# Kernel optimization log

Measured on AMD Instinct MI355X. Metric: run time of the kernel, lower is better.

The kernel has to match this reference:

```python
import jax, jax.numpy as jnp
import numpy as np

EDGE_FEAT_DIM = 128
N_HEADS = 8


def setup_inputs() -> dict:
    key = jax.random.key(0)
    k1, k2, k3, k4 = jax.random.split(key, 4)
    E = 131072
    N = 4096
    edge_index = jax.random.randint(k1, (2, E), 0, N, dtype=jnp.int64)
    edge_attr = jax.random.normal(k2, (E, EDGE_FEAT_DIM), dtype=jnp.float32)
    # Linear(edge_feat_dim, n_heads) params (PyTorch default init scale)
    bound = 1.0 / np.sqrt(EDGE_FEAT_DIM)
    W = jax.random.uniform(k3, (EDGE_FEAT_DIM, N_HEADS), jnp.float32, -bound, bound)
    b = jax.random.uniform(k4, (N_HEADS,), jnp.float32, -bound, bound)
    return {"edge_index": edge_index, "edge_attr": edge_attr, "num_nodes": N,
            "W": W, "b": b}


def reference(edge_index, edge_attr, num_nodes, W, b):
    N = num_nodes
    # proj: (E, n_heads) — small GEMM
    proj = edge_attr @ W + b
    i = edge_index[0]
    j = edge_index[1]
    # In-range mask (original skips out-of-range indices; here all in-range,
    # but keep the semantics faithful).
    valid = (i >= 0) & (i < N) & (j >= 0) & (j < N)
    proj = jnp.where(valid[:, None], proj, 0.0)
    i = jnp.clip(i, 0, N - 1)
    j = jnp.clip(j, 0, N - 1)
    # Scatter-add into dense (N, N, n_heads) bias
    bias = jnp.zeros((N, N, proj.shape[-1]), dtype=proj.dtype)
    bias = bias.at[i, j].add(proj)
    return bias
```

## Files before the change

### kernel.cpp

```cpp
#include <hip/hip_runtime.h>


__global__ __launch_bounds__(256) void efe_scatter_kernel(
    const int* __restrict__ ei,
    const float* __restrict__ attr,
    const int* __restrict__ nn,
    const float* __restrict__ Wm,
    const float* __restrict__ bv,
    float* __restrict__ out,
    int E)
{
    const int N = nn[0];
    const int tid    = blockIdx.x * blockDim.x + threadIdx.x;
    const int wave   = tid >> 6;
    const int lane   = threadIdx.x & 63;
    const int lg     = lane & 15;
    const int sub    = lane >> 4;
    const int nwaves = (gridDim.x * blockDim.x) >> 6;

    float w[2][4][8];
#pragma unroll
    for (int half = 0; half < 2; ++half)
#pragma unroll
        for (int c = 0; c < 4; ++c) {
            const int k = half * 64 + lg * 4 + c;
#pragma unroll
            for (int h = 0; h < 8; ++h) w[half][c][h] = Wm[k * 8 + h];
        }
    float bh[8];
#pragma unroll
    for (int h = 0; h < 8; ++h) bh[h] = bv[h];

    const int nquads = (E + 3) >> 2;
    for (int q = wave; q < nquads; q += nwaves) {
        const int e = q * 4 + sub;
        float acc[8];
#pragma unroll
        for (int h = 0; h < 8; ++h) acc[h] = 0.f;

        const bool live = (e < E);
        if (live) {
            const float4* row = (const float4*)(attr + (size_t)e * 128);
#pragma unroll
            for (int half = 0; half < 2; ++half) {
                const float4 v = row[half * 16 + lg];
#pragma unroll
                for (int h = 0; h < 8; ++h)
                    acc[h] += v.x * w[half][0][h] + v.y * w[half][1][h]
                            + v.z * w[half][2][h] + v.w * w[half][3][h];
            }
        }
#pragma unroll
        for (int d = 1; d < 16; d <<= 1)
#pragma unroll
            for (int h = 0; h < 8; ++h)
                acc[h] += __shfl_xor(acc[h], d, 64);

        if (live && lg < 8) {
            const int i = ei[e];
            const int j = ei[E + e];
            if (i >= 0 && i < N && j >= 0 && j < N) {
                float v = acc[0] + bh[0];
#pragma unroll
                for (int h = 1; h < 8; ++h) {
                    const float cand = acc[h] + bh[h];
                    v = (lg == h) ? cand : v;
                }
                atomicAdd(out + (((size_t)i * N + j) << 3) + lg, v);
            }
        }
    }
}

extern "C" void kernel_launch(void* const* d_in, const int* in_sizes, int n_in,
                              void* d_out, int out_size, void* d_ws, size_t ws_size,
                              hipStream_t stream) {
    const int*   ei   = (const int*)d_in[0];
    const float* attr = (const float*)d_in[1];
    const int*   nn   = (const int*)d_in[2];
    const float* Wm   = (const float*)d_in[3];
    const float* bv   = (const float*)d_in[4];
    float*       out  = (float*)d_out;

    const int E = in_sizes[0] / 2;

    hipMemsetAsync(d_out, 0, (size_t)out_size * sizeof(float), stream);

    efe_scatter_kernel<<<2048, 256, 0, stream>>>(ei, attr, nn, Wm, bv, out, E);
}
```

Measured before the change: 128.5 us.

## Bin edges by output chunk and fuse zero-fill with scatter accumulation

Replaces the full-output memset and scattered global atomics with a two-pass scheme. The first kernel computes the projections into a workspace and bins edge ids into 1024-cell chunks using per-chunk counters. The second kernel writes each output chunk exactly once, accumulating binned contributions in registers and handling overflow with atomics. This removes the separate memset pass and most atomics on the large 512MB output. In exchange it needs workspace, more kernels, and a serial per-block record loop, and the overflow path scans every overflow record in every block.

```diff
diff --git a/kernel.cpp b/kernel.cpp
--- a/kernel.cpp
+++ b/kernel.cpp
@@ -1,13 +1,21 @@
 #include <hip/hip_runtime.h>
-
-
-__global__ __launch_bounds__(256) void efe_scatter_kernel(
+#include <math.h>
+
+
+#define CHUNK_CELLS 1024
+#define BIN_CAP     64
+
+__global__ __launch_bounds__(256) void efe_proj_bin_kernel(
     const int* __restrict__ ei,
     const float* __restrict__ attr,
     const int* __restrict__ nn,
     const float* __restrict__ Wm,
     const float* __restrict__ bv,
-    float* __restrict__ out,
+    float* __restrict__ proj,
+    unsigned* __restrict__ counters,
+    unsigned* __restrict__ bins,
+    unsigned* __restrict__ ocnt,
+    unsigned long long* __restrict__ ovf,
     int E)
 {
     const int N = nn[0];
@@ -34,11 +42,15 @@
     const int nquads = (E + 3) >> 2;
     for (int q = wave; q < nquads; q += nwaves) {
         const int e = q * 4 + sub;
+        const bool live = (e < E);
+
+        int i = 0, j = 0;
+        if (live) { i = ei[e]; j = ei[E + e]; }
+
         float acc[8];
 #pragma unroll
         for (int h = 0; h < 8; ++h) acc[h] = 0.f;
 
-        const bool live = (e < E);
         if (live) {
             const float4* row = (const float4*)(attr + (size_t)e * 128);
 #pragma unroll
@@ -57,17 +69,152 @@
                 acc[h] += __shfl_xor(acc[h], d, 64);
 
         if (live && lg < 8) {
-            const int i = ei[e];
-            const int j = ei[E + e];
+            float v = acc[0] + bh[0];
+#pragma unroll
+            for (int h = 1; h < 8; ++h) {
+                const float cand = acc[h] + bh[h];
+                v = (lg == h) ? cand : v;
+            }
+            proj[(size_t)e * 8 + lg] = v;
+        }
+        if (live && lg == 0) {
             if (i >= 0 && i < N && j >= 0 && j < N) {
-                float v = acc[0] + bh[0];
-#pragma unroll
-                for (int h = 1; h < 8; ++h) {
-                    const float cand = acc[h] + bh[h];
-                    v = (lg == h) ? cand : v;
+                const long cell = (long)i * N + j;
+                const unsigned chunk = (unsigned)(cell >> 10);
+                const unsigned lc    = (unsigned)(cell & 1023u);
+                const unsigned pos = atomicAdd(&counters[chunk], 1u);
+                if (pos < BIN_CAP)
+                    bins[(size_t)chunk * BIN_CAP + pos] = (lc << 20) | (unsigned)e;
+                else {
+                    const unsigned op = atomicAdd(ocnt, 1u);
+                    ovf[op] = ((unsigned long long)cell << 32) | (unsigned)e;
                 }
-                atomicAdd(out + (((size_t)i * N + j) << 3) + lg, v);
-            }
+            }
+        }
+    }
+}
+
+__global__ __launch_bounds__(256) void efe_fill_inject_kernel(
+    const unsigned* __restrict__ counters,
+    const unsigned* __restrict__ bins,
+    const unsigned* __restrict__ ocnt,
+    const unsigned long long* __restrict__ ovf,
+    const float* __restrict__ proj,
+    float* __restrict__ out)
+{
+    const unsigned chunk = blockIdx.x;
+    const int t = threadIdx.x;
+
+    float4 acc[8];
+#pragma unroll
+    for (int k = 0; k < 8; ++k) acc[k] = make_float4(0.f, 0.f, 0.f, 0.f);
+
+    unsigned cnt = counters[chunk];
+    if (cnt > BIN_CAP) cnt = BIN_CAP;
+    const unsigned* mybins = bins + (size_t)chunk * BIN_CAP;
+
+    for (unsigned r = 0; r < cnt; ++r) {
+        const unsigned rec = mybins[r];
+        const int lc = (int)(rec >> 20);
+        const unsigned e = rec & 0xFFFFFu;
+        const int f0 = lc << 1, f1 = f0 | 1;
+        if ((f0 & 255) == t) {
+            const float4 p = *(const float4*)(proj + (size_t)e * 8);
+            const int k = f0 >> 8;
+#pragma unroll
+            for (int kk = 0; kk < 8; ++kk)
+                if (kk == k) { acc[kk].x += p.x; acc[kk].y += p.y;
+                               acc[kk].z += p.z; acc[kk].w += p.w; }
+        }
+        if ((f1 & 255) == t) {
+            const float4 p = *(const float4*)(proj + (size_t)e * 8 + 4);
+            const int k = f1 >> 8;
+#pragma unroll
+            for (int kk = 0; kk < 8; ++kk)
+                if (kk == k) { acc[kk].x += p.x; acc[kk].y += p.y;
+                               acc[kk].z += p.z; acc[kk].w += p.w; }
+        }
+    }
+
+    float4* out4 = (float4*)out + (size_t)chunk * (CHUNK_CELLS * 8 / 4);
+#pragma unroll
+    for (int k = 0; k < 8; ++k) out4[(size_t)k * 256 + t] = acc[k];
+
+    const unsigned oc = *ocnt;
+    if (oc) {
+        __threadfence();
+        __syncthreads();
+        if (t < 8) {
+            for (unsigned o = 0; o < oc; ++o) {
+                const unsigned long long rec = ovf[o];
+                const long cell = (long)(rec >> 32);
+                const unsigned e = (unsigned)(rec & 0xFFFFFFFFu);
+                if ((unsigned)(cell >> 10) == chunk)
+                    atomicAdd(out + (size_t)cell * 8 + t, proj[(size_t)e * 8 + t]);
+            }
+        }
+    }
+}
+
+__global__ __launch_bounds__(256) void efe_scatter_kernel(
+    const int* __restrict__ ei, const float* __restrict__ attr,
+    const int* __restrict__ nn, const float* __restrict__ Wm,
+    const float* __restrict__ bv, float* __restrict__ out, int E)
+{
+    const int N = nn[0];
+    const int tid    = blockIdx.x * blockDim.x + threadIdx.x;
+    const int wave   = tid >> 6;
+    const int lane   = threadIdx.x & 63;
+    const int lg     = lane & 15;
+    const int sub    = lane >> 4;
+    const int nwaves = (gridDim.x * blockDim.x) >> 6;
+
+    float w[2][4][8];
+#pragma unroll
+    for (int half = 0; half < 2; ++half)
+#pragma unroll
+        for (int c = 0; c < 4; ++c) {
+            const int k = half * 64 + lg * 4 + c;
+#pragma unroll
+            for (int h = 0; h < 8; ++h) w[half][c][h] = Wm[k * 8 + h];
+        }
+    float bh[8];
+#pragma unroll
+    for (int h = 0; h < 8; ++h) bh[h] = bv[h];
+
+    const int nquads = (E + 3) >> 2;
+    for (int q = wave; q < nquads; q += nwaves) {
+        const int e = q * 4 + sub;
+        const bool live = (e < E);
+        int i = 0, j = 0;
+        if (live) { i = ei[e]; j = ei[E + e]; }
+        float acc[8];
+#pragma unroll
+        for (int h = 0; h < 8; ++h) acc[h] = 0.f;
+        if (live) {
+            const float4* row = (const float4*)(attr + (size_t)e * 128);
+#pragma unroll
+            for (int half = 0; half < 2; ++half) {
+                const float4 v = row[half * 16 + lg];
+#pragma unroll
+                for (int h = 0; h < 8; ++h)
+                    acc[h] += v.x * w[half][0][h] + v.y * w[half][1][h]
+                            + v.z * w[half][2][h] + v.w * w[half][3][h];
+            }
+        }
+#pragma unroll
+        for (int d = 1; d < 16; d <<= 1)
+#pragma unroll
+            for (int h = 0; h < 8; ++h)
+                acc[h] += __shfl_xor(acc[h], d, 64);
+        if (live && lg < 8 && i >= 0 && i < N && j >= 0 && j < N) {
+            float v = acc[0] + bh[0];
+#pragma unroll
+            for (int h = 1; h < 8; ++h) {
+                const float cand = acc[h] + bh[h];
+                v = (lg == h) ? cand : v;
+            }
+            atomicAdd(out + (((size_t)i * N + j) << 3) + lg, v);
         }
     }
 }
@@ -84,7 +231,35 @@
 
     const int E = in_sizes[0] / 2;
 
-    hipMemsetAsync(d_out, 0, (size_t)out_size * sizeof(float), stream);
-
-    efe_scatter_kernel<<<2048, 256, 0, stream>>>(ei, attr, nn, Wm, bv, out, E);
-}
+    const long ncells = (long)out_size / 8;
+    const long Nh = (long)(sqrt((double)ncells) + 0.5);
+    const bool shape_ok = (Nh * Nh == ncells) && (ncells % CHUNK_CELLS == 0) &&
+                          (E > 0) && (E <= (1 << 20));
+
+    const size_t nchunks = (size_t)(ncells / CHUNK_CELLS);
+    const size_t o_cnt  = 0;
+    const size_t o_ocnt = nchunks * 4;
+    const size_t o_ovf  = ((o_ocnt + 4 + 255) / 256) * 256;
+    const size_t o_proj = ((o_ovf + (size_t)E * 8 + 255) / 256) * 256;
+    const size_t o_bins = ((o_proj + (size_t)E * 32 + 255) / 256) * 256;
+    const size_t need   = o_bins + nchunks * BIN_CAP * 4;
+
+    if (shape_ok && ws_size >= need) {
+        unsigned* counters = (unsigned*)((char*)d_ws + o_cnt);
+        unsigned* ocnt     = (unsigned*)((char*)d_ws + o_ocnt);
+        unsigned long long* ovf = (unsigned long long*)((char*)d_ws + o_ovf);
+        float*    proj     = (float*)((char*)d_ws + o_proj);
+        unsigned* bins     = (unsigned*)((char*)d_ws + o_bins);
+
+        hipMemsetAsync(d_ws, 0, o_ovf, stream);
+
+        efe_proj_bin_kernel<<<2048, 256, 0, stream>>>(
+            ei, attr, nn, Wm, bv, proj, counters, bins, ocnt, ovf, E);
+
+        efe_fill_inject_kernel<<<(unsigned)nchunks, 256, 0, stream>>>(
+            counters, bins, ocnt, ovf, proj, out);
+    } else {
+        hipMemsetAsync(d_out, 0, (size_t)out_size * sizeof(float), stream);
+        efe_scatter_kernel<<<2048, 256, 0, stream>>>(ei, attr, nn, Wm, bv, out, E);
+    }
+}
```

After: 152.9 us. +18.9%, slower.
